# Performance work log

Hardware: AMD Instinct MI355X
Metric: run time of the kernel (lower is better)

## Reference

```python
import jax, jax.numpy as jnp
import numpy as np

B, S, H, V = 256, 15, 512, 50257

def setup_inputs() -> dict:
    key = jax.random.key(0)
    ks = jax.random.split(key, 12)
    sc_h = 1.0 / np.sqrt(H)
    sc_in = 1.0 / np.sqrt(2 * H)
    return {
        "input_tokens": jax.random.randint(ks[0], (B, 1), 0, V),
        "hidden": jax.random.normal(ks[1], (1, B, H), jnp.float32),
        "encoder_outputs": jax.random.normal(ks[2], (B, S, H), jnp.float32),
        "emb_table": jax.random.normal(ks[3], (V, H), jnp.float32),
        "attn_W": jax.random.uniform(ks[4], (H, H), jnp.float32, -sc_h, sc_h),
        "attn_b": jax.random.uniform(ks[5], (H,), jnp.float32, -sc_h, sc_h),
        "W_ih": jax.random.uniform(ks[6], (3 * H, 2 * H), jnp.float32, -sc_in, sc_in),
        "W_hh": jax.random.uniform(ks[7], (3 * H, H), jnp.float32, -sc_h, sc_h),
        "b_ih": jax.random.uniform(ks[8], (3 * H,), jnp.float32, -sc_h, sc_h),
        "b_hh": jax.random.uniform(ks[9], (3 * H,), jnp.float32, -sc_h, sc_h),
        "out_W": jax.random.uniform(ks[10], (V, H), jnp.float32, -sc_h, sc_h),
        "out_b": jax.random.uniform(ks[11], (V,), jnp.float32, -sc_h, sc_h),
    }


def reference(input_tokens, hidden, encoder_outputs, emb_table, attn_W, attn_b,
              W_ih, W_hh, b_ih, b_hh, out_W, out_b):
    # Embedding (dropout is identity in eval/reference mode): [B,1,H]
    embedded = emb_table[input_tokens]
    h = hidden[0]  # [B,H]

    # Bahdanau-style scores, vectorized over the seq dim instead of the python loop:
    # energies[b,s] = attn(enc[b,s]);  score[b,s] = <h[b], energies[b,s]>
    energies = jnp.einsum("bsh,oh->bso", encoder_outputs, attn_W) + attn_b  # [B,S,H]
    attn_scores = jnp.einsum("bso,bo->bs", energies, h)                      # [B,S]
    attn_weights = jax.nn.softmax(attn_scores, axis=1)                       # [B,S]

    # context = weights @ encoder_outputs: [B,1,H]
    context = jnp.einsum("bs,bsh->bh", attn_weights, encoder_outputs)[:, None, :]

    # GRU single step (PyTorch gate order: r, z, n)
    x = jnp.concatenate([embedded, context], axis=2)[:, 0]  # [B,2H]
    gi = x @ W_ih.T + b_ih   # [B,3H]
    gh = h @ W_hh.T + b_hh   # [B,3H]
    i_r, i_z, i_n = jnp.split(gi, 3, axis=1)
    h_r, h_z, h_n = jnp.split(gh, 3, axis=1)
    r = jax.nn.sigmoid(i_r + h_r)
    z = jax.nn.sigmoid(i_z + h_z)
    n = jnp.tanh(i_n + r * h_n)
    h_new = (1.0 - z) * n + z * h            # [B,H]

    logits = h_new[:, None, :] @ out_W.T + out_b   # [B,1,V]
    log_probs = jax.nn.log_softmax(logits, axis=-1)
    return log_probs, h_new[None], attn_weights
```

## Files before the change

kernel.cpp:

```cpp
#include <hip/hip_runtime.h>

#define V_SIZE 50257
#define B_SIZE 256
#define S_LEN  15
#define H_DIM  512
#define NBLK_LG 786

typedef __attribute__((ext_vector_type(8))) short bf16x8;
typedef __attribute__((ext_vector_type(4))) float f32x4;

__device__ __forceinline__ unsigned short f2bf(float f) {
    unsigned int u = __float_as_uint(f);
    u += 0x7fffu + ((u >> 16) & 1u);
    return (unsigned short)(u >> 16);
}

__global__ __launch_bounds__(256) void u_kernel(
    const float* __restrict__ hidden, const float* __restrict__ attn_W,
    float* __restrict__ u)
{
    __shared__ float h_s[16][H_DIM];
    const int tid = threadIdx.x;
    const int b0 = blockIdx.y * 16, n0 = blockIdx.x * 32;
    const float4* hv = (const float4*)(hidden + (size_t)b0 * H_DIM);
    float4* hs4 = (float4*)&h_s[0][0];
    #pragma unroll
    for (int i = 0; i < 8; ++i) hs4[tid + i * 256] = hv[tid + i * 256];
    __syncthreads();
    const int n = n0 + (tid & 31);
    const int m = (tid >> 5) * 2;
    float a0 = 0.f, a1 = 0.f;
    #pragma unroll 8
    for (int o = 0; o < H_DIM; ++o) {
        float w = attn_W[(size_t)o * H_DIM + n];
        a0 += h_s[m][o] * w;
        a1 += h_s[m + 1][o] * w;
    }
    u[(size_t)(b0 + m) * H_DIM + n] = a0;
    u[(size_t)(b0 + m + 1) * H_DIM + n] = a1;
}

__global__ __launch_bounds__(256) void attn_kernel(
    const float* __restrict__ hidden, const float* __restrict__ enc,
    const float* __restrict__ u, const int* __restrict__ tokens,
    const float* __restrict__ emb, float* __restrict__ attnw_out,
    unsigned short* __restrict__ x_bf, unsigned short* __restrict__ h_bf)
{
    const int b = blockIdx.x, tid = threadIdx.x;
    __shared__ float e_s[S_LEN][H_DIM];
    __shared__ float u_s[H_DIM];
    __shared__ float sc_s[S_LEN];
    __shared__ float w_s[S_LEN];
    {
        const float4* ev = (const float4*)(enc + (size_t)b * S_LEN * H_DIM);
        float4* es4 = (float4*)&e_s[0][0];
        #pragma unroll
        for (int i = 0; i < 8; ++i) {
            int idx = i * 256 + tid;
            if (idx < S_LEN * H_DIM / 4) es4[idx] = ev[idx];
        }
    }
    u_s[tid]       = u[(size_t)b * H_DIM + tid];
    u_s[tid + 256] = u[(size_t)b * H_DIM + tid + 256];
    h_bf[(size_t)b * H_DIM + tid]       = f2bf(hidden[(size_t)b * H_DIM + tid]);
    h_bf[(size_t)b * H_DIM + tid + 256] = f2bf(hidden[(size_t)b * H_DIM + tid + 256]);
    const int tok = tokens[b];
    x_bf[(size_t)b * 2 * H_DIM + tid]       = f2bf(emb[(size_t)tok * H_DIM + tid]);
    x_bf[(size_t)b * 2 * H_DIM + tid + 256] = f2bf(emb[(size_t)tok * H_DIM + tid + 256]);
    __syncthreads();
    const int wave = tid >> 6, lane = tid & 63;
    for (int s = wave; s < S_LEN; s += 4) {
        float acc = 0.f;
        #pragma unroll
        for (int k = 0; k < H_DIM / 64; ++k)
            acc += e_s[s][lane + k * 64] * u_s[lane + k * 64];
        #pragma unroll
        for (int off = 32; off; off >>= 1) acc += __shfl_down(acc, off);
        if (lane == 0) sc_s[s] = acc;
    }
    __syncthreads();
    float mx = -1e30f;
    for (int s = 0; s < S_LEN; ++s) mx = fmaxf(mx, sc_s[s]);
    float sum = 0.f;
    for (int s = 0; s < S_LEN; ++s) sum += __expf(sc_s[s] - mx);
    const float inv = 1.f / sum;
    if (tid < S_LEN) {
        float w = __expf(sc_s[tid] - mx) * inv;
        w_s[tid] = w;
        attnw_out[b * S_LEN + tid] = w;
    }
    __syncthreads();
    #pragma unroll
    for (int hh = 0; hh < 2; ++hh) {
        int h = tid + hh * 256;
        float c = 0.f;
        #pragma unroll
        for (int s = 0; s < S_LEN; ++s)
            c += w_s[s] * e_s[s][h];
        x_bf[(size_t)b * 2 * H_DIM + H_DIM + h] = f2bf(c);
    }
}

struct GemmP {
    const unsigned short* A; const float* B; const float* bias; float* C;
    int N; int K;
};

template<int BM, int BN, int BK, int WR, int WC>
__global__ __launch_bounds__(256) void gemm_nt(GemmP p0, GemmP p1)
{
    GemmP p = (blockIdx.z == 0) ? p0 : p1;
    constexpr int LDA = BK + 8;
    __shared__ __align__(16) unsigned short As[BM][LDA];
    __shared__ __align__(16) unsigned short Bs[BN][LDA];
    const int tid = threadIdx.x;
    const int bn0 = blockIdx.x * BN;
    const int bm0 = blockIdx.y * BM;
    const int wave = tid >> 6, lane = tid & 63;
    const int wm = (wave / WC) * (BM / WR);
    const int wn = (wave % WC) * (BN / WC);
    constexpr int MF = BM / WR / 16, NF = BN / WC / 16;
    const int n16 = lane & 15, quad = lane >> 4;

    f32x4 acc[MF][NF] = {};

    for (int k0 = 0; k0 < p.K; k0 += BK) {
        #pragma unroll
        for (int it = 0; it < BM / 32; ++it) {
            int v = it * 256 + tid;
            int row = v >> 3, seg = v & 7;
            *(uint4*)&As[row][seg * 8] =
                *(const uint4*)(p.A + (size_t)(bm0 + row) * p.K + k0 + seg * 8);
        }
        #pragma unroll
        for (int it = 0; it < BN / 32; ++it) {
            int v = it * 256 + tid;
            int row = v >> 3, seg = v & 7;
            int gv = bn0 + row;
            float4 w0 = make_float4(0, 0, 0, 0), w1 = make_float4(0, 0, 0, 0);
            if (gv < p.N) {
                const float4* src = (const float4*)(p.B + (size_t)gv * p.K + k0 + seg * 8);
                w0 = src[0]; w1 = src[1];
            }
            uint4 pk;
            pk.x = (unsigned)f2bf(w0.x) | ((unsigned)f2bf(w0.y) << 16);
            pk.y = (unsigned)f2bf(w0.z) | ((unsigned)f2bf(w0.w) << 16);
            pk.z = (unsigned)f2bf(w1.x) | ((unsigned)f2bf(w1.y) << 16);
            pk.w = (unsigned)f2bf(w1.z) | ((unsigned)f2bf(w1.w) << 16);
            *(uint4*)&Bs[row][seg * 8] = pk;
        }
        __syncthreads();
        #pragma unroll
        for (int kk = 0; kk < BK; kk += 32) {
            bf16x8 af[MF], bfr[NF];
            #pragma unroll
            for (int i = 0; i < MF; ++i)
                af[i] = *(const bf16x8*)&As[wm + i * 16 + n16][kk + quad * 8];
            #pragma unroll
            for (int j = 0; j < NF; ++j)
                bfr[j] = *(const bf16x8*)&Bs[wn + j * 16 + n16][kk + quad * 8];
            #pragma unroll
            for (int i = 0; i < MF; ++i)
                #pragma unroll
                for (int j = 0; j < NF; ++j)
                    acc[i][j] = __builtin_amdgcn_mfma_f32_16x16x32_bf16(
                        af[i], bfr[j], acc[i][j], 0, 0, 0);
        }
        __syncthreads();
    }
    #pragma unroll
    for (int i = 0; i < MF; ++i) {
        const int r0 = bm0 + wm + i * 16 + quad * 4;
        #pragma unroll
        for (int j = 0; j < NF; ++j) {
            const int c = bn0 + wn + j * 16 + n16;
            if (c < p.N) {
                const float bv = p.bias[c];
                #pragma unroll
                for (int r = 0; r < 4; ++r)
                    p.C[(size_t)(r0 + r) * p.N + c] = acc[i][j][r] + bv;
            }
        }
    }
}

template<bool PART>
__global__ __launch_bounds__(256, 4) void gemm_lg(
    const unsigned short* __restrict__ A, const float* __restrict__ B,
    const float* __restrict__ bias, float* __restrict__ C,
    float* __restrict__ pm, float* __restrict__ ps)
{
    constexpr int BN = 64, BK = 128;
    constexpr int LDB = BK + 8;
    __shared__ __align__(16) unsigned short Bs[BN][LDB];
    const int tid = threadIdx.x;
    const int blk = blockIdx.x;
    int bx, by;
    if (blk < 1568) { int g = blk >> 4, s = blk & 15; bx = g * 8 + (s & 7); by = s >> 3; }
    else            { int s = blk - 1568;             bx = 784 + (s >> 1);  by = s & 1;  }
    const int bn0 = bx * BN;
    const int m0  = by * 128;
    const int wave = tid >> 6, lane = tid & 63;
    const int wm = wave * 32;
    const int n16 = lane & 15, quad = lane >> 4;

    f32x4 acc[2][4] = {};
    const unsigned short* arow[2];
    #pragma unroll
    for (int i = 0; i < 2; ++i)
        arow[i] = A + (size_t)(m0 + wm + i * 16 + n16) * H_DIM;

    for (int k0 = 0; k0 < H_DIM; k0 += BK) {
        #pragma unroll
        for (int it = 0; it < 4; ++it) {
            int v = it * 256 + tid;
            int row = v >> 4, seg = v & 15;
            int gv = bn0 + row;
            float4 w0 = make_float4(0, 0, 0, 0), w1 = make_float4(0, 0, 0, 0);
            if (gv < V_SIZE) {
                const float4* src = (const float4*)(B + (size_t)gv * H_DIM + k0 + seg * 8);
                w0 = src[0]; w1 = src[1];
            }
            uint4 pk;
            pk.x = (unsigned)f2bf(w0.x) | ((unsigned)f2bf(w0.y) << 16);
            pk.y = (unsigned)f2bf(w0.z) | ((unsigned)f2bf(w0.w) << 16);
            pk.z = (unsigned)f2bf(w1.x) | ((unsigned)f2bf(w1.y) << 16);
            pk.w = (unsigned)f2bf(w1.z) | ((unsigned)f2bf(w1.w) << 16);
            *(uint4*)&Bs[row][seg * 8] = pk;
        }
        __syncthreads();
        #pragma unroll
        for (int kk = 0; kk < BK; kk += 32) {
            bf16x8 af[2], bfr[4];
            #pragma unroll
            for (int i = 0; i < 2; ++i)
                af[i] = *(const bf16x8*)(arow[i] + k0 + kk + quad * 8);
            #pragma unroll
            for (int j = 0; j < 4; ++j)
                bfr[j] = *(const bf16x8*)&Bs[j * 16 + n16][kk + quad * 8];
            #pragma unroll
            for (int i = 0; i < 2; ++i)
                #pragma unroll
                for (int j = 0; j < 4; ++j)
                    acc[i][j] = __builtin_amdgcn_mfma_f32_16x16x32_bf16(
                        af[i], bfr[j], acc[i][j], 0, 0, 0);
        }
        __syncthreads();
    }

    int cj[4]; float bvv[4]; bool okj[4];
    #pragma unroll
    for (int j = 0; j < 4; ++j) {
        cj[j] = bn0 + j * 16 + n16;
        okj[j] = cj[j] < V_SIZE;
        bvv[j] = okj[j] ? bias[cj[j]] : 0.f;
    }
    #pragma unroll
    for (int i = 0; i < 2; ++i) {
        const int r0 = wm + i * 16 + quad * 4;
        if (PART) {
            #pragma unroll
            for (int r = 0; r < 4; ++r) {
                float m = -1e30f;
                #pragma unroll
                for (int j = 0; j < 4; ++j)
                    if (okj[j]) m = fmaxf(m, acc[i][j][r] + bvv[j]);
                #pragma unroll
                for (int d = 1; d < 16; d <<= 1) m = fmaxf(m, __shfl_xor(m, d));
                float s = 0.f;
                #pragma unroll
                for (int j = 0; j < 4; ++j)
                    if (okj[j]) s += __expf(acc[i][j][r] + bvv[j] - m);
                #pragma unroll
                for (int d = 1; d < 16; d <<= 1) s += __shfl_xor(s, d);
                if (n16 == 0) {
                    pm[(size_t)bx * B_SIZE + m0 + r0 + r] = m;
                    ps[(size_t)bx * B_SIZE + m0 + r0 + r] = s;
                }
            }
        }
        #pragma unroll
        for (int j = 0; j < 4; ++j) if (okj[j]) {
            #pragma unroll
            for (int r = 0; r < 4; ++r)
                C[(size_t)(m0 + r0 + r) * V_SIZE + cj[j]] = acc[i][j][r] + bvv[j];
        }
    }
}

__global__ __launch_bounds__(256) void gru_kernel(
    const float* __restrict__ gi, const float* __restrict__ gh,
    const float* __restrict__ hidden, float* __restrict__ hnew_out,
    unsigned short* __restrict__ hnew_bf)
{
    const int idx = blockIdx.x * 256 + threadIdx.x;
    const int b = idx >> 9, h = idx & 511;
    const float* gib = gi + (size_t)b * 3 * H_DIM;
    const float* ghb = gh + (size_t)b * 3 * H_DIM;
    float r = 1.f / (1.f + __expf(-(gib[h] + ghb[h])));
    float z = 1.f / (1.f + __expf(-(gib[H_DIM + h] + ghb[H_DIM + h])));
    float n = gib[2 * H_DIM + h] + r * ghb[2 * H_DIM + h];
    n = 1.f - 2.f / (1.f + __expf(2.f * n));
    float hp = hidden[idx];
    float hn = (1.f - z) * n + z * hp;
    hnew_out[idx] = hn;
    hnew_bf[idx] = f2bf(hn);
}

__global__ __launch_bounds__(1024) void finalize_kernel(
    float* __restrict__ logits, const float* __restrict__ pm,
    const float* __restrict__ ps)
{
    const int b = blockIdx.x, tid = threadIdx.x;
    float m = -1e30f, s = 0.f;
    for (int i = tid; i < NBLK_LG; i += 1024) {
        float mm = pm[(size_t)i * B_SIZE + b], ss = ps[(size_t)i * B_SIZE + b];
        float nm = fmaxf(m, mm);
        s = s * __expf(m - nm) + ss * __expf(mm - nm);
        m = nm;
    }
    const int lane = tid & 63, wave = tid >> 6;
    #pragma unroll
    for (int off = 32; off; off >>= 1) {
        float m2 = __shfl_down(m, off), s2 = __shfl_down(s, off);
        float nm = fmaxf(m, m2);
        s = s * __expf(m - nm) + s2 * __expf(m2 - nm);
        m = nm;
    }
    __shared__ float msh[16], ssh[16], lse_sh;
    if (lane == 0) { msh[wave] = m; ssh[wave] = s; }
    __syncthreads();
    if (tid == 0) {
        float M = msh[0], S = ssh[0];
        for (int w = 1; w < 16; ++w) {
            float nm = fmaxf(M, msh[w]);
            S = S * __expf(M - nm) + ssh[w] * __expf(msh[w] - nm);
            M = nm;
        }
        lse_sh = M + logf(S);
    }
    __syncthreads();
    const float lse = lse_sh;
    constexpr int HALF = 25132;
    const int start = blockIdx.y * HALF;
    const int end = min(V_SIZE, start + HALF);
    float* p0 = logits + (size_t)b * V_SIZE + start;
    const int n = end - start;
    const int mis = (int)(((uintptr_t)p0 >> 2) & 3);
    int pre = mis ? (4 - mis) : 0; if (pre > n) pre = n;
    if (tid < pre) p0[tid] -= lse;
    const int nvec = (n - pre) >> 2;
    float4* rv = (float4*)(p0 + pre);
    for (int i = tid; i < nvec; i += 1024) {
        float4 v = rv[i];
        v.x -= lse; v.y -= lse; v.z -= lse; v.w -= lse;
        rv[i] = v;
    }
    const int rem = n - pre - (nvec << 2);
    if (tid < rem) p0[pre + (nvec << 2) + tid] -= lse;
}

__global__ __launch_bounds__(1024) void logsoftmax_kernel(float* __restrict__ logits)
{
    const int b = blockIdx.x, tid = threadIdx.x;
    float* row = logits + (size_t)b * V_SIZE;
    float m = -1e30f, s = 0.f;
    for (int c = tid; c < V_SIZE; c += 1024) {
        float x = row[c];
        float nm = fmaxf(m, x);
        s = s * __expf(m - nm) + __expf(x - nm);
        m = nm;
    }
    const int lane = tid & 63, wave = tid >> 6;
    #pragma unroll
    for (int off = 32; off; off >>= 1) {
        float m2 = __shfl_down(m, off), s2 = __shfl_down(s, off);
        float nm = fmaxf(m, m2);
        s = s * __expf(m - nm) + s2 * __expf(m2 - nm);
        m = nm;
    }
    __shared__ float msh[16], ssh[16], lse_sh;
    if (lane == 0) { msh[wave] = m; ssh[wave] = s; }
    __syncthreads();
    if (tid == 0) {
        float M = msh[0], S = ssh[0];
        for (int w = 1; w < 16; ++w) {
            float nm = fmaxf(M, msh[w]);
            S = S * __expf(M - nm) + ssh[w] * __expf(msh[w] - nm);
            M = nm;
        }
        lse_sh = M + logf(S);
    }
    __syncthreads();
    const float lse = lse_sh;
    for (int c = tid; c < V_SIZE; c += 1024) row[c] -= lse;
}

constexpr size_t OFF_U      = 0;
constexpr size_t OFF_XBF    = 524288;
constexpr size_t OFF_HBF    = 1048576;
constexpr size_t OFF_HNEWBF = 1310720;
constexpr size_t OFF_GI     = 1572864;
constexpr size_t OFF_GH     = 3145728;
constexpr size_t OFF_PM     = 4718592;
constexpr size_t OFF_PS     = 5523456;
constexpr size_t WS_NEED    = 6328320;

extern "C" void kernel_launch(void* const* d_in, const int* in_sizes, int n_in,
                              void* d_out, int out_size, void* d_ws, size_t ws_size,
                              hipStream_t stream) {
    const int*   tokens = (const int*)d_in[0];
    const float* hidden = (const float*)d_in[1];
    const float* enc    = (const float*)d_in[2];
    const float* emb    = (const float*)d_in[3];
    const float* attn_W = (const float*)d_in[4];
    const float* W_ih   = (const float*)d_in[6];
    const float* W_hh   = (const float*)d_in[7];
    const float* b_ih   = (const float*)d_in[8];
    const float* b_hh   = (const float*)d_in[9];
    const float* out_W  = (const float*)d_in[10];
    const float* out_b  = (const float*)d_in[11];

    float* out = (float*)d_out;
    float* logp      = out;
    float* hnew_out  = out + (size_t)B_SIZE * V_SIZE;
    float* attnw_out = hnew_out + (size_t)B_SIZE * H_DIM;

    char* ws = (char*)d_ws;
    float*          u_ws    = (float*)(ws + OFF_U);
    unsigned short* x_bf    = (unsigned short*)(ws + OFF_XBF);
    unsigned short* h_bf    = (unsigned short*)(ws + OFF_HBF);
    unsigned short* hnew_bf = (unsigned short*)(ws + OFF_HNEWBF);
    float*          gi_ws   = (float*)(ws + OFF_GI);
    float*          gh_ws   = (float*)(ws + OFF_GH);
    float*          pm_ws   = (float*)(ws + OFF_PM);
    float*          ps_ws   = (float*)(ws + OFF_PS);

    u_kernel<<<dim3(16, 16), 256, 0, stream>>>(hidden, attn_W, u_ws);
    attn_kernel<<<dim3(256), 256, 0, stream>>>(hidden, enc, u_ws, tokens, emb,
                                               attnw_out, x_bf, h_bf);
    GemmP gi_p { x_bf, W_ih, b_ih, gi_ws, 3 * H_DIM, 2 * H_DIM };
    GemmP gh_p { h_bf, W_hh, b_hh, gh_ws, 3 * H_DIM, H_DIM };
    gemm_nt<64, 64, 64, 2, 2><<<dim3(24, 4, 2), 256, 0, stream>>>(gi_p, gh_p);
    gru_kernel<<<dim3(512), 256, 0, stream>>>(gi_ws, gh_ws, hidden, hnew_out, hnew_bf);

    if (ws_size >= WS_NEED) {
        gemm_lg<true><<<dim3(2 * NBLK_LG), 256, 0, stream>>>(
            hnew_bf, out_W, out_b, logp, pm_ws, ps_ws);
        finalize_kernel<<<dim3(256, 2), 1024, 0, stream>>>(logp, pm_ws, ps_ws);
    } else {
        gemm_lg<false><<<dim3(2 * NBLK_LG), 256, 0, stream>>>(
            hnew_bf, out_W, out_b, logp, nullptr, nullptr);
        logsoftmax_kernel<<<dim3(256), 1024, 0, stream>>>(logp);
    }
}
```

Before: 366.1 us.

## Fuse attention projection into attn kernel and split vocab GEMM launch

Result: no change. 368.8 us (+0.7%).

```diff
diff --git a/kernel.cpp b/kernel.cpp
--- a/kernel.cpp
+++ b/kernel.cpp
@@ -15,39 +15,15 @@
     return (unsigned short)(u >> 16);
 }
 
-__global__ __launch_bounds__(256) void u_kernel(
-    const float* __restrict__ hidden, const float* __restrict__ attn_W,
-    float* __restrict__ u)
-{
-    __shared__ float h_s[16][H_DIM];
-    const int tid = threadIdx.x;
-    const int b0 = blockIdx.y * 16, n0 = blockIdx.x * 32;
-    const float4* hv = (const float4*)(hidden + (size_t)b0 * H_DIM);
-    float4* hs4 = (float4*)&h_s[0][0];
-    #pragma unroll
-    for (int i = 0; i < 8; ++i) hs4[tid + i * 256] = hv[tid + i * 256];
-    __syncthreads();
-    const int n = n0 + (tid & 31);
-    const int m = (tid >> 5) * 2;
-    float a0 = 0.f, a1 = 0.f;
-    #pragma unroll 8
-    for (int o = 0; o < H_DIM; ++o) {
-        float w = attn_W[(size_t)o * H_DIM + n];
-        a0 += h_s[m][o] * w;
-        a1 += h_s[m + 1][o] * w;
-    }
-    u[(size_t)(b0 + m) * H_DIM + n] = a0;
-    u[(size_t)(b0 + m + 1) * H_DIM + n] = a1;
-}
-
 __global__ __launch_bounds__(256) void attn_kernel(
     const float* __restrict__ hidden, const float* __restrict__ enc,
-    const float* __restrict__ u, const int* __restrict__ tokens,
-    const float* __restrict__ emb, float* __restrict__ attnw_out,
+    const int* __restrict__ tokens, const float* __restrict__ emb,
+    const float* __restrict__ attn_W, float* __restrict__ attnw_out,
     unsigned short* __restrict__ x_bf, unsigned short* __restrict__ h_bf)
 {
     const int b = blockIdx.x, tid = threadIdx.x;
     __shared__ float e_s[S_LEN][H_DIM];
+    __shared__ float h_sh[H_DIM];
     __shared__ float u_s[H_DIM];
     __shared__ float sc_s[S_LEN];
     __shared__ float w_s[S_LEN];
@@ -60,13 +36,25 @@
             if (idx < S_LEN * H_DIM / 4) es4[idx] = ev[idx];
         }
     }
-    u_s[tid]       = u[(size_t)b * H_DIM + tid];
-    u_s[tid + 256] = u[(size_t)b * H_DIM + tid + 256];
-    h_bf[(size_t)b * H_DIM + tid]       = f2bf(hidden[(size_t)b * H_DIM + tid]);
-    h_bf[(size_t)b * H_DIM + tid + 256] = f2bf(hidden[(size_t)b * H_DIM + tid + 256]);
+    const float hv0 = hidden[(size_t)b * H_DIM + tid];
+    const float hv1 = hidden[(size_t)b * H_DIM + tid + 256];
+    h_sh[tid] = hv0; h_sh[tid + 256] = hv1;
+    h_bf[(size_t)b * H_DIM + tid]       = f2bf(hv0);
+    h_bf[(size_t)b * H_DIM + tid + 256] = f2bf(hv1);
     const int tok = tokens[b];
     x_bf[(size_t)b * 2 * H_DIM + tid]       = f2bf(emb[(size_t)tok * H_DIM + tid]);
     x_bf[(size_t)b * 2 * H_DIM + tid + 256] = f2bf(emb[(size_t)tok * H_DIM + tid + 256]);
+    __syncthreads();
+    {
+        float u0 = 0.f, u1 = 0.f;
+        #pragma unroll 8
+        for (int o = 0; o < H_DIM; ++o) {
+            const float hs = h_sh[o];
+            u0 += hs * attn_W[(size_t)o * H_DIM + tid];
+            u1 += hs * attn_W[(size_t)o * H_DIM + tid + 256];
+        }
+        u_s[tid] = u0; u_s[tid + 256] = u1;
+    }
     __syncthreads();
     const int wave = tid >> 6, lane = tid & 63;
     for (int s = wave; s < S_LEN; s += 4) {
@@ -188,7 +176,7 @@
 __global__ __launch_bounds__(256, 4) void gemm_lg(
     const unsigned short* __restrict__ A, const float* __restrict__ B,
     const float* __restrict__ bias, float* __restrict__ C,
-    float* __restrict__ pm, float* __restrict__ ps)
+    float* __restrict__ pm, float* __restrict__ ps, int bx0)
 {
     constexpr int BN = 64, BK = 128;
     constexpr int LDB = BK + 8;
@@ -196,8 +184,8 @@
     const int tid = threadIdx.x;
     const int blk = blockIdx.x;
     int bx, by;
-    if (blk < 1568) { int g = blk >> 4, s = blk & 15; bx = g * 8 + (s & 7); by = s >> 3; }
-    else            { int s = blk - 1568;             bx = 784 + (s >> 1);  by = s & 1;  }
+    if (blk < 784) { int g = blk >> 4, s = blk & 15; bx = bx0 + g * 8 + (s & 7); by = s >> 3; }
+    else           { int s = blk - 784;              bx = bx0 + 392;             by = s;      }
     const int bn0 = bx * BN;
     const int m0  = by * 128;
     const int wave = tid >> 6, lane = tid & 63;
@@ -427,7 +415,6 @@
     float* attnw_out = hnew_out + (size_t)B_SIZE * H_DIM;
 
     char* ws = (char*)d_ws;
-    float*          u_ws    = (float*)(ws + OFF_U);
     unsigned short* x_bf    = (unsigned short*)(ws + OFF_XBF);
     unsigned short* h_bf    = (unsigned short*)(ws + OFF_HBF);
     unsigned short* hnew_bf = (unsigned short*)(ws + OFF_HNEWBF);
@@ -436,8 +423,7 @@
     float*          pm_ws   = (float*)(ws + OFF_PM);
     float*          ps_ws   = (float*)(ws + OFF_PS);
 
-    u_kernel<<<dim3(16, 16), 256, 0, stream>>>(hidden, attn_W, u_ws);
-    attn_kernel<<<dim3(256), 256, 0, stream>>>(hidden, enc, u_ws, tokens, emb,
+    attn_kernel<<<dim3(256), 256, 0, stream>>>(hidden, enc, tokens, emb, attn_W,
                                                attnw_out, x_bf, h_bf);
     GemmP gi_p { x_bf, W_ih, b_ih, gi_ws, 3 * H_DIM, 2 * H_DIM };
     GemmP gh_p { h_bf, W_hh, b_hh, gh_ws, 3 * H_DIM, H_DIM };
@@ -445,12 +431,16 @@
     gru_kernel<<<dim3(512), 256, 0, stream>>>(gi_ws, gh_ws, hidden, hnew_out, hnew_bf);
 
     if (ws_size >= WS_NEED) {
-        gemm_lg<true><<<dim3(2 * NBLK_LG), 256, 0, stream>>>(
-            hnew_bf, out_W, out_b, logp, pm_ws, ps_ws);
+        gemm_lg<true><<<dim3(NBLK_LG), 256, 0, stream>>>(
+            hnew_bf, out_W, out_b, logp, pm_ws, ps_ws, 0);
+        gemm_lg<true><<<dim3(NBLK_LG), 256, 0, stream>>>(
+            hnew_bf, out_W, out_b, logp, pm_ws, ps_ws, 393);
         finalize_kernel<<<dim3(256, 2), 1024, 0, stream>>>(logp, pm_ws, ps_ws);
     } else {
-        gemm_lg<false><<<dim3(2 * NBLK_LG), 256, 0, stream>>>(
-            hnew_bf, out_W, out_b, logp, nullptr, nullptr);
+        gemm_lg<false><<<dim3(NBLK_LG), 256, 0, stream>>>(
+            hnew_bf, out_W, out_b, logp, nullptr, nullptr, 0);
+        gemm_lg<false><<<dim3(NBLK_LG), 256, 0, stream>>>(
+            hnew_bf, out_W, out_b, logp, nullptr, nullptr, 393);
         logsoftmax_kernel<<<dim3(256), 1024, 0, stream>>>(logp);
     }
 }
```
